# Kernel tuning notes

Hardware: AMD Instinct MI355X
Metric: run time of the kernel (lower is better)

## Reference

```python
import jax, jax.numpy as jnp
import numpy as np

# Detect() defaults from the source
NUM_CLASSES = 2
TOP_K = 750          # max detections returned per class
NMS_TOP_K = 5000     # candidates considered by NMS
NMS_THRESH = 0.3
CONF_THRESH = 0.05
VAR0, VAR1 = 0.1, 0.2  # prior box variances


def decode(loc, priors):
    # loc, priors: [P,4]; priors in (cx,cy,w,h); returns corner boxes [P,4]
    xy = priors[:, :2] + loc[:, :2] * VAR0 * priors[:, 2:]
    wh = priors[:, 2:] * jnp.exp(loc[:, 2:] * VAR1)
    x1y1 = xy - wh * 0.5
    x2y2 = x1y1 + wh
    return jnp.concatenate([x1y1, x2y2], axis=1)


def nms_single(boxes, scores):
    # boxes [P,4], scores [P] -> kept rows [TOP_K,5] = (score, x1,y1,x2,y2)
    s = jnp.where(scores > CONF_THRESH, scores, -1.0)
    top_s, top_i = jax.lax.top_k(s, NMS_TOP_K)   # restrict to best nms_top_k candidates
    cb = boxes[top_i]                             # [K,4] candidate boxes
    area = (cb[:, 2] - cb[:, 0]) * (cb[:, 3] - cb[:, 1])
    ar = jnp.arange(NMS_TOP_K)

    def step(s_cur, _):
        i = jnp.argmax(s_cur)                     # highest-scoring unsuppressed box
        sc = s_cur[i]
        ok = sc > 0.0                             # any valid candidate left?
        b = cb[i]
        xx1 = jnp.maximum(cb[:, 0], b[0])
        yy1 = jnp.maximum(cb[:, 1], b[1])
        xx2 = jnp.minimum(cb[:, 2], b[2])
        yy2 = jnp.minimum(cb[:, 3], b[3])
        inter = jnp.clip(xx2 - xx1, 0.0) * jnp.clip(yy2 - yy1, 0.0)
        union = area - inter + area[i]
        iou = inter / union
        supp = (iou > NMS_THRESH) | (ar == i)     # suppress overlapping + self
        s_next = jnp.where(ok & supp, -1.0, s_cur)
        row = jnp.where(ok, jnp.concatenate([sc[None], b]), jnp.zeros(5, boxes.dtype))
        return s_next, row

    _, rows = jax.lax.scan(step, top_s, None, length=TOP_K)
    return rows  # [TOP_K, 5]


def setup_inputs() -> dict:
    key = jax.random.key(0)
    k1, k2, k3 = jax.random.split(key, 3)
    B, P = 8, 136500
    loc_data = jax.random.normal(k1, (B, P, 4), jnp.float32)
    conf_data = jax.random.normal(k2, (B, P, 2), jnp.float32)
    u = jax.random.uniform(k3, (P, 4), jnp.float32)
    # priors: cx,cy in (0,1); w,h small positive (normalized coords)
    prior_data = jnp.concatenate([u[:, :2], u[:, 2:] * 0.1 + 0.01], axis=1)
    return {"loc_data": loc_data, "conf_data": conf_data, "prior_data": prior_data}


def reference(loc_data, conf_data, prior_data):
    B = loc_data.shape[0]
    conf = jax.nn.softmax(conf_data, axis=-1)                    # [B,P,2]
    boxes = jax.vmap(lambda l: decode(l, prior_data))(loc_data)  # [B,P,4]
    rows = jax.vmap(nms_single)(boxes, conf[:, :, 1])            # [B,TOP_K,5]
    out = jnp.zeros((B, NUM_CLASSES, TOP_K, 5), loc_data.dtype)  # class 0 = background, all zeros
    out = out.at[:, 1].set(rows)
    return out
```

## Files before the change

### kernel.cpp

```cpp
#include <hip/hip_runtime.h>
#include <stdint.h>

#pragma clang fp contract(off)

#define NPRI   136500
#define BATCH  8
#define NMS_K  5000
#define NKPAD  5120
#define TOPK   750
#define SORT_N 8192
#define HBINS  1024
#define HOFF   0x3D40
#define MROW   80
#define CNTSTRIDE 32
#define CUT    32

typedef unsigned long long u64;

__device__ __forceinline__ u64 shfl64(u64 v, int src) {
    int lo = __shfl((int)(unsigned)(v & 0xffffffffull), src);
    int hi = __shfl((int)(unsigned)(v >> 32), src);
    return ((u64)(unsigned)hi << 32) | (u64)(unsigned)lo;
}
__device__ __forceinline__ u64 shfl64_xor(u64 v, int m) {
    int lo = __shfl_xor((int)(unsigned)(v & 0xffffffffull), m);
    int hi = __shfl_xor((int)(unsigned)(v >> 32), m);
    return ((u64)(unsigned)hi << 32) | (u64)(unsigned)lo;
}

__device__ __forceinline__ bool iou_sup(float4 c4, float aj,
                                        float4 rbx, float ra) {
    float xx1 = fmaxf(c4.x, rbx.x);
    float yy1 = fmaxf(c4.y, rbx.y);
    float xx2 = fminf(c4.z, rbx.z);
    float yy2 = fminf(c4.w, rbx.w);
    float iw = fmaxf(xx2 - xx1, 0.0f);
    float ih = fmaxf(yy2 - yy1, 0.0f);
    float inter = iw * ih;
    float uni = (aj - inter) + ra;
    float u = fmaf(-0.3f, uni, inter);
    float d = fmaf(-1.4901161193847656e-8f, uni, u);
    return d > 0.0f;
}
__device__ __forceinline__ u64 iou_word(float4 c4, float aj,
                                        float4 rbx, float ra) {
    return __ballot(iou_sup(c4, aj, rbx, ra));
}

__device__ __forceinline__ u64 diag_mask(u64 word, int sh) {
    if (sh >= 0)
        word &= (sh >= 63) ? 0ull : (~0ull << (sh + 1));
    return word;
}

__device__ u64 row_word_slow(const float4* __restrict__ cbp,
                             const float* __restrict__ cap,
                             float4 rbx, float ra, int W) {
    int jbase = W << 6;
    u64 word = 0ull;
    for (int jj = 0; jj < 64; ++jj) {
        int jc = min(jbase + jj, NMS_K - 1);
        if (iou_sup(cbp[jc], cap[jc], rbx, ra)) word |= (1ull << jj);
    }
    return word;
}

__global__ __launch_bounds__(256) void score_hist_kernel(
        const float* __restrict__ conf, unsigned int* __restrict__ hist,
        float* __restrict__ sraw) {
    int b = blockIdx.y;
    __shared__ unsigned int h[HBINS];
    for (int i = threadIdx.x; i < HBINS; i += 256) h[i] = 0;
    __syncthreads();
    for (int p = blockIdx.x * 256 + threadIdx.x; p < NPRI; p += 64 * 256) {
        float2 c = ((const float2*)conf)[(size_t)b * NPRI + p];
        float m  = fmaxf(c.x, c.y);
        float e0 = expf(c.x - m), e1 = expf(c.y - m);
        float s  = e1 / (e0 + e1);
        sraw[(size_t)b * NPRI + p] = s;
        if (s > 0.05f) {
            int bin = (int)(__float_as_uint(s) >> 16) - HOFF;
            bin = min(max(bin, 0), HBINS - 1);
            atomicAdd(&h[bin], 1u);
        }
    }
    __syncthreads();
    for (int i = threadIdx.x; i < HBINS; i += 256) {
        unsigned int v = h[i];
        if (v) atomicAdd(&hist[b * HBINS + i], v);
    }
}

__global__ __launch_bounds__(256) void compact_kernel(
        const float* __restrict__ sraw, const unsigned int* __restrict__ hist,
        u64* __restrict__ keys, unsigned int* __restrict__ cnt) {
    int b = blockIdx.y;
    int tid = threadIdx.x;
    int lane = tid & 63;
    __shared__ u64 buf[2304];
    __shared__ unsigned int hsum[256];
    __shared__ int best_sh;
    __shared__ unsigned int nloc;
    __shared__ unsigned int base_sh;
    const unsigned int* hb = hist + b * HBINS;
    int t4 = tid * 4;
    unsigned int h0 = hb[t4], h1 = hb[t4 + 1], h2 = hb[t4 + 2], h3 = hb[t4 + 3];
    hsum[tid] = h0 + h1 + h2 + h3;
    if (tid == 0) { best_sh = 0; nloc = 0; }
    __syncthreads();
    for (int o = 1; o < 256; o <<= 1) {
        unsigned int add = (tid + o < 256) ? hsum[tid + o] : 0u;
        __syncthreads();
        hsum[tid] += add;
        __syncthreads();
    }
    unsigned int nxt = (tid + 1 < 256) ? hsum[tid + 1] : 0u;
    unsigned int s3 = h3 + nxt;
    unsigned int s2 = h2 + s3;
    unsigned int s1 = h1 + s2;
    unsigned int s0 = h0 + s1;
    int cand = -1;
    if (s3 >= (unsigned)NMS_K) cand = t4 + 3;
    else if (s2 >= (unsigned)NMS_K) cand = t4 + 2;
    else if (s1 >= (unsigned)NMS_K) cand = t4 + 1;
    else if (s0 >= (unsigned)NMS_K) cand = t4;
    if (cand > 0) atomicMax(&best_sh, cand);
    __syncthreads();
    int tb = best_sh;
    for (int p = blockIdx.x * 256 + tid; p < NPRI; p += 64 * 256) {
        float s = sraw[(size_t)b * NPRI + p];
        bool pass = false;
        unsigned int bits = 0;
        if (s > 0.05f) {
            bits = __float_as_uint(s);
            int bin = (int)(bits >> 16) - HOFF;
            bin = min(max(bin, 0), HBINS - 1);
            pass = (bin >= tb);
        }
        u64 bal = __ballot(pass);
        int rank = (int)__popcll(bal & ((1ull << lane) - 1ull));
        unsigned int wbase = 0;
        if (lane == 0 && bal)
            wbase = atomicAdd(&nloc, (unsigned)__popcll(bal));
        wbase = (unsigned)__shfl((int)wbase, 0);
        if (pass)
            buf[wbase + rank] = ((u64)bits << 32) | (u64)(~(unsigned int)p);
    }
    __syncthreads();
    unsigned int tot = nloc;
    if (tid == 0)
        base_sh = tot ? atomicAdd(&cnt[b * CNTSTRIDE], tot) : 0u;
    __syncthreads();
    unsigned int base = base_sh;
    for (unsigned int i = tid; i < tot; i += 256) {
        unsigned int pos = base + i;
        if (pos < SORT_N)
            keys[(size_t)b * SORT_N + pos] = buf[i];
    }
}

__global__ __launch_bounds__(512) void sort2k_kernel(
        const u64* __restrict__ keys, u64* __restrict__ keys2,
        const unsigned int* __restrict__ cnt) {
    int b = blockIdx.y, c = blockIdx.x;
    int tid = threadIdx.x;
    int n = min((int)cnt[b * CNTSTRIDE], SORT_N);
    int base = c * 2048;
    if (base >= n) {
        for (int i = tid; i < 2048; i += 512)
            keys2[(size_t)b * SORT_N + base + i] = 0ull;
        return;
    }
    __shared__ u64 k[2048];
    for (int i = tid; i < 2048; i += 512)
        k[i] = (base + i < n) ? keys[(size_t)b * SORT_N + base + i] : 0ull;
    __syncthreads();
    for (int kk = 2; kk <= 2048; kk <<= 1) {
        bool top = (kk == 2048);
        for (int j = kk >> 1; j > 0; j >>= 1) {
            for (int i = tid; i < 2048; i += 512) {
                int ixj = i ^ j;
                if (ixj > i) {
                    u64 a = k[i], v = k[ixj];
                    bool desc = top || ((i & kk) == 0);
                    if (desc ? (a < v) : (a > v)) { k[i] = v; k[ixj] = a; }
                }
            }
            __syncthreads();
        }
    }
    for (int i = tid; i < 2048; i += 512)
        keys2[(size_t)b * SORT_N + base + i] = k[i];
}

__global__ __launch_bounds__(256) void merge1_kernel(
        const u64* __restrict__ keys2, u64* __restrict__ keys) {
    int b = blockIdx.y;
    int o = blockIdx.x * 256 + threadIdx.x;
    int pair = o >> 12;
    int oo = o & 4095;
    const u64* A  = keys2 + (size_t)b * SORT_N + pair * 4096;
    const u64* Bp = A + 2048;
    int lo = max(0, oo - 2048), hi = min(oo, 2048);
    while (lo < hi) {
        int mid = (lo + hi + 1) >> 1;
        bool ok = (oo - mid >= 2048) || (A[mid - 1] >= Bp[oo - mid]);
        if (ok) lo = mid; else hi = mid - 1;
    }
    int i = lo, j = oo - lo;
    u64 v;
    if (j >= 2048) v = A[i];
    else if (i >= 2048) v = Bp[j];
    else v = (A[i] >= Bp[j]) ? A[i] : Bp[j];
    keys[(size_t)b * SORT_N + pair * 4096 + oo] = v;
}

__global__ __launch_bounds__(256) void merge2_decode_kernel(
        const u64* __restrict__ keys,
        const float* __restrict__ loc, const float* __restrict__ priors,
        float* __restrict__ cscore, float* __restrict__ cbox,
        float* __restrict__ carea) {
    int b = blockIdx.y;
    int o = blockIdx.x * 256 + threadIdx.x;
    const u64* A  = keys + (size_t)b * SORT_N;
    const u64* Bp = A + 4096;
    int lo = max(0, o - 4096), hi = min(o, 4096);
    while (lo < hi) {
        int mid = (lo + hi + 1) >> 1;
        bool ok = (o - mid >= 4096) || (A[mid - 1] >= Bp[o - mid]);
        if (ok) lo = mid; else hi = mid - 1;
    }
    int i = lo, j = o - lo;
    u64 key;
    if (j >= 4096) key = A[i];
    else if (i >= 4096) key = Bp[j];
    else key = (A[i] >= Bp[j]) ? A[i] : Bp[j];
    if (o >= NMS_K) return;
    float sc; int idx;
    if (key != 0ull) {
        sc  = __uint_as_float((unsigned int)(key >> 32));
        idx = (int)(~(unsigned int)key);
    } else { sc = -1.0f; idx = 0; }
    cscore[b * NMS_K + o] = sc;
    float x1 = 0.f, y1 = 0.f, x2 = 0.f, y2 = 0.f, ar = 0.f;
    if (key != 0ull) {
        const float* l  = loc + ((size_t)b * NPRI + idx) * 4;
        const float* pr = priors + (size_t)idx * 4;
        float lx = l[0], ly = l[1], lw = l[2], lh = l[3];
        float pcx = pr[0], pcy = pr[1], pw = pr[2], ph = pr[3];
        float cx = pcx + (lx * 0.1f) * pw;
        float cy = pcy + (ly * 0.1f) * ph;
        float wd = pw * expf(lw * 0.2f);
        float ht = ph * expf(lh * 0.2f);
        x1 = cx - wd * 0.5f;  y1 = cy - ht * 0.5f;
        x2 = x1 + wd;         y2 = y1 + ht;
        ar = (x2 - x1) * (y2 - y1);
    }
    float* cb = cbox + ((size_t)b * NMS_K + o) * 4;
    cb[0] = x1; cb[1] = y1; cb[2] = x2; cb[3] = y2;
    carea[b * NMS_K + o] = ar;
}

__global__ __launch_bounds__(256, 4) void maskbuild_kernel(
        const float* __restrict__ cbox, const float* __restrict__ carea,
        u64* __restrict__ M) {
    int b   = blockIdx.y;
    int bid = blockIdx.x;
    int wgq, rb;
    if (bid >= 380) { wgq = 19; rb = bid - 380; }
    else {
        int w = (int)((sqrtf((float)(4 * bid + 5)) - 1.0f) * 0.5f);
        while (w * (w + 1) > bid) w--;
        while ((w + 1) * (w + 2) <= bid) w++;
        wgq = w; rb = bid - w * (w + 1);
    }
    int tid  = threadIdx.x;
    int lane = tid & 63;
    int wv   = __builtin_amdgcn_readfirstlane(tid >> 6);
    int w0   = wgq * 4;
    int rowbase = rb * 128;

    __shared__ float4 rbox[128];
    __shared__ float  rarea[128];
    if (tid < 128) {
        int i  = rowbase + tid;
        int ic = min(i, NMS_K - 1);
        rbox[tid]  = ((const float4*)cbox)[(size_t)b * NMS_K + ic];
        rarea[tid] = carea[(size_t)b * NMS_K + ic];
    }
    const float4* __restrict__ cbp = (const float4*)cbox + (size_t)b * NMS_K;
    const float*  __restrict__ cap = carea + (size_t)b * NMS_K;
    int j0 = w0 * 64 + lane;
    float4 c4_0 = cbp[min(j0,       NMS_K - 1)];
    float4 c4_1 = cbp[min(j0 +  64, NMS_K - 1)];
    float4 c4_2 = cbp[min(j0 + 128, NMS_K - 1)];
    float4 c4_3 = cbp[min(j0 + 192, NMS_K - 1)];
    float aj0 = cap[min(j0,       NMS_K - 1)];
    float aj1 = cap[min(j0 +  64, NMS_K - 1)];
    float aj2 = cap[min(j0 + 128, NMS_K - 1)];
    float aj3 = cap[min(j0 + 192, NMS_K - 1)];
    __syncthreads();

    int lr0 = 32 * wv;
    int rglob0 = rowbase + lr0;
    if (rglob0 >= NMS_K) return;

    u64* __restrict__ Mb = M + (size_t)b * NKPAD * MROW;

    if (rglob0 + 31 < w0 * 64) {
#pragma unroll 2
        for (int q = 0; q < 32; q += 2) {
            int lr = lr0 + q;
            float4 rb0 = rbox[lr], rb1 = rbox[lr + 1];
            float  ra0 = rarea[lr], ra1 = rarea[lr + 1];
            u64 A0 = iou_word(c4_0, aj0, rb0, ra0);
            u64 B0 = iou_word(c4_0, aj0, rb1, ra1);
            u64 A1 = iou_word(c4_1, aj1, rb0, ra0);
            u64 B1 = iou_word(c4_1, aj1, rb1, ra1);
            u64 A2 = iou_word(c4_2, aj2, rb0, ra0);
            u64 B2 = iou_word(c4_2, aj2, rb1, ra1);
            u64 A3 = iou_word(c4_3, aj3, rb0, ra0);
            u64 B3 = iou_word(c4_3, aj3, rb1, ra1);
            int row0 = rglob0 + q;
            if (lane == 0) {
                u64* d0 = Mb + (size_t)row0 * MROW + w0;
                ((ulonglong2*)d0)[0] = make_ulonglong2(A0, A1);
                ((ulonglong2*)d0)[1] = make_ulonglong2(A2, A3);
                u64* d1 = d0 + MROW;
                ((ulonglong2*)d1)[0] = make_ulonglong2(B0, B1);
                ((ulonglong2*)d1)[1] = make_ulonglong2(B2, B3);
            }
        }
    } else {
        int nrows = min(32, NMS_K - rglob0);
        int sh_base = rglob0 - w0 * 64;
#pragma unroll 2
        for (int q = 0; q < nrows; q += 2) {
            int lr = lr0 + q;
            float4 rb0 = rbox[lr], rb1 = rbox[lr + 1];
            float  ra0 = rarea[lr], ra1 = rarea[lr + 1];
            u64 A0 = iou_word(c4_0, aj0, rb0, ra0);
            u64 B0 = iou_word(c4_0, aj0, rb1, ra1);
            u64 A1 = iou_word(c4_1, aj1, rb0, ra0);
            u64 B1 = iou_word(c4_1, aj1, rb1, ra1);
            u64 A2 = iou_word(c4_2, aj2, rb0, ra0);
            u64 B2 = iou_word(c4_2, aj2, rb1, ra1);
            u64 A3 = iou_word(c4_3, aj3, rb0, ra0);
            u64 B3 = iou_word(c4_3, aj3, rb1, ra1);
            int sh = sh_base + q;
            A0 = diag_mask(A0, sh);       B0 = diag_mask(B0, sh + 1);
            A1 = diag_mask(A1, sh - 64);  B1 = diag_mask(B1, sh - 63);
            A2 = diag_mask(A2, sh - 128); B2 = diag_mask(B2, sh - 127);
            A3 = diag_mask(A3, sh - 192); B3 = diag_mask(B3, sh - 191);
            int row0 = rglob0 + q;
            if (lane == 0) {
                u64* d0 = Mb + (size_t)row0 * MROW + w0;
                ((ulonglong2*)d0)[0] = make_ulonglong2(A0, A1);
                ((ulonglong2*)d0)[1] = make_ulonglong2(A2, A3);
                u64* d1 = d0 + MROW;
                ((ulonglong2*)d1)[0] = make_ulonglong2(B0, B1);
                ((ulonglong2*)d1)[1] = make_ulonglong2(B2, B3);
            }
        }
    }
}

__global__ __launch_bounds__(1024) void maskscan_kernel(
        const float* __restrict__ cscore, const float* __restrict__ cbox,
        const float* __restrict__ carea,
        const unsigned int* __restrict__ cnt, const u64* __restrict__ M,
        float* __restrict__ out) {
    int b = blockIdx.x;
    int tid = threadIdx.x, lane = tid & 63, wv = tid >> 6;
    int nv = min((int)cnt[b * CNTSTRIDE], NMS_K);
    const u64* MB = M + (size_t)b * NKPAD * MROW;
    const float4* __restrict__ cbp = (const float4*)cbox + (size_t)b * NMS_K;
    const float*  __restrict__ cap = carea + (size_t)b * NMS_K;
    float* outb = out + (size_t)b * 2 * TOPK * 5;
    __shared__ unsigned int supp4[4];
    __shared__ u64 dbuf[2][64];
    __shared__ short allp[TOPK];
    __shared__ int emitted_sh;
    for (int i = tid; i < 2 * TOPK * 5; i += 1024) outb[i] = 0.f;
    if (tid < 4) supp4[tid] = 0u;
    if (tid == 0) emitted_sh = 0;
    if (wv == 1) dbuf[0][lane] = MB[(size_t)lane * MROW];
    __syncthreads();
    int emitted = 0;
    int nwords = (nv + 63) >> 6;
    u64 colw_prev = 0ull;
    u64 pickprev  = 0ull;
    for (int w = 0; w < nwords; w++) {
        int par = w & 1;
        if (wv == 0) {
            u64 colw;
            if (w + 1 < CUT) {
                colw = MB[(size_t)(w * 64 + lane) * MROW + (w + 1)];
            } else {
                int rc = min(w * 64 + lane, NMS_K - 1);
                colw = row_word_slow(cbp, cap, cbp[rc], cap[rc], w + 1);
            }
            u64 D = dbuf[par][lane];
            u64 sup = ((u64)supp4[2 * par + 1] << 32) | (u64)supp4[2 * par];
            if (lane == 0) {
                supp4[2 * par] = 0u;
                supp4[2 * par + 1] = 0u;
            }
            u64 x = ((pickprev >> lane) & 1ull) ? colw_prev : 0ull;
#pragma unroll
            for (int m = 1; m < 64; m <<= 1) x |= shfl64_xor(x, m);
            sup |= x;
            int base = w * 64, rem = nv - base;
            u64 valid = (rem >= 64) ? ~0ull : ((1ull << rem) - 1ull);
            u64 alive = valid & ~sup;
            u64 nz = __ballot(D != 0ull);
            u64 pickmask = 0ull;
            while (alive) {
                u64 blockers = alive & nz;
                if (!blockers) { pickmask |= alive; break; }
                int nb = __builtin_ctzll(blockers);
                u64 mle = (nb >= 63) ? ~0ull : ((1ull << (nb + 1)) - 1ull);
                pickmask |= alive & mle;
                u64 rw = shfl64(D, nb);
                alive &= ~mle;
                alive &= ~rw;
            }
            int room = TOPK - emitted;
            int pc = __popcll(pickmask);
            while (pc > room) {
                pickmask &= ~(1ull << (63 - __builtin_clzll(pickmask)));
                pc--;
            }
            if (lane == 0) emitted_sh = emitted + pc;
            if ((pickmask >> lane) & 1ull) {
                int rank = (int)__popcll(pickmask & ((1ull << lane) - 1ull));
                allp[emitted + rank] = (short)(base + lane);
            }
            pickprev = pickmask;
            colw_prev = colw;
        } else if (wv == 1) {
            if (w + 1 < nwords) {
                int W = w + 1;
                u64 dpre;
                if (W < CUT) {
                    dpre = MB[(size_t)(W * 64 + lane) * MROW + W];
                } else {
                    int rc = min(W * 64 + lane, NMS_K - 1);
                    dpre = diag_mask(
                        row_word_slow(cbp, cap, cbp[rc], cap[rc], W), lane);
                }
                dbuf[W & 1][lane] = dpre;
            }
        } else {
            int i = (wv - 2) * 64 + lane;
            u64 v = 0ull;
            if (i < emitted) {
                int pr = allp[i];
                if (w + 1 < CUT)
                    v = MB[(size_t)pr * MROW + (w + 1)];
                else
                    v = row_word_slow(cbp, cap, cbp[pr], cap[pr], w + 1);
            }
#pragma unroll
            for (int m = 1; m < 64; m <<= 1) v |= shfl64_xor(v, m);
            if (lane == 0 && v) {
                atomicOr(&supp4[2 * (par ^ 1)],     (unsigned int)v);
                atomicOr(&supp4[2 * (par ^ 1) + 1], (unsigned int)(v >> 32));
            }
        }
        __syncthreads();
        emitted = emitted_sh;
        if (emitted >= TOPK) break;
    }
    for (int t = tid; t < emitted; t += 1024) {
        int p = allp[t];
        float sc  = cscore[b * NMS_K + p];
        float4 bx = ((const float4*)cbox)[(size_t)b * NMS_K + p];
        float* o = outb + (size_t)(TOPK + t) * 5;
        o[0] = sc; o[1] = bx.x; o[2] = bx.y; o[3] = bx.z; o[4] = bx.w;
    }
}

extern "C" void kernel_launch(void* const* d_in, const int* in_sizes, int n_in,
                              void* d_out, int out_size, void* d_ws, size_t ws_size,
                              hipStream_t stream) {
    const float* loc    = (const float*)d_in[0];
    const float* conf   = (const float*)d_in[1];
    const float* priors = (const float*)d_in[2];
    float* out = (float*)d_out;

    char* ws = (char*)d_ws;
    size_t off = 0;
    unsigned int* hist = (unsigned int*)(ws + off);   off += (size_t)BATCH * HBINS * 4;
    unsigned int* cnt  = (unsigned int*)(ws + off);   off += (size_t)BATCH * CNTSTRIDE * 4;
    size_t zero_bytes = off;
    u64* keys  = (u64*)(ws + off);                    off += (size_t)BATCH * SORT_N * 8;
    u64* keys2 = (u64*)(ws + off);                    off += (size_t)BATCH * SORT_N * 8;
    float* cscore = (float*)(ws + off);               off += (size_t)BATCH * NMS_K * 4;
    float* cbox   = (float*)(ws + off);               off += (size_t)BATCH * NMS_K * 16;
    float* carea  = (float*)(ws + off);               off += (size_t)BATCH * NMS_K * 4;
    u64* M = (u64*)(ws + off);                        off += (size_t)BATCH * NKPAD * MROW * 8;
    float* sraw = (float*)M;

    hipMemsetAsync(d_ws, 0, zero_bytes, stream);

    score_hist_kernel<<<dim3(64, BATCH), 256, 0, stream>>>(conf, hist, sraw);
    compact_kernel<<<dim3(64, BATCH), 256, 0, stream>>>(sraw, hist, keys, cnt);
    sort2k_kernel<<<dim3(4, BATCH), 512, 0, stream>>>(keys, keys2, cnt);
    merge1_kernel<<<dim3(32, BATCH), 256, 0, stream>>>(keys2, keys);
    merge2_decode_kernel<<<dim3(20, BATCH), 256, 0, stream>>>(keys, loc, priors, cscore, cbox, carea);
    maskbuild_kernel<<<dim3(72, BATCH), 256, 0, stream>>>(cbox, carea, M);
    maskscan_kernel<<<BATCH, 1024, 0, stream>>>(cscore, cbox, carea, cnt, M, out);
}
```

Before: 185.0 us.

## Replace shared-memory bitonic sort with wave-shuffle sort plus merge-path passes

The 2048-element per-block bitonic sort, which needed a block barrier at every one of its many stages, is replaced. Each wave now sorts 64-element chunks in registers with xor shuffles, and five merge-path passes ping-pong between two shared buffers to combine them, with one barrier per pass. This cuts the number of block-wide synchronisations and shared-memory round trips. In exchange it adds binary-search work per output element and doubles the shared memory used per block.

```diff
diff --git a/kernel.cpp b/kernel.cpp
--- a/kernel.cpp
+++ b/kernel.cpp
@@ -159,11 +159,13 @@
     }
 }
 
-__global__ __launch_bounds__(512) void sort2k_kernel(
+__global__ __launch_bounds__(512) void sortmerge2k_kernel(
         const u64* __restrict__ keys, u64* __restrict__ keys2,
         const unsigned int* __restrict__ cnt) {
     int b = blockIdx.y, c = blockIdx.x;
     int tid = threadIdx.x;
+    int lane = tid & 63;
+    int wv = tid >> 6;
     int n = min((int)cnt[b * CNTSTRIDE], SORT_N);
     int base = c * 2048;
     if (base >= n) {
@@ -172,25 +174,51 @@
         return;
     }
     __shared__ u64 k[2048];
+    __shared__ u64 k2[2048];
+    for (int ch = wv; ch < 32; ch += 8) {
+        int idx = base + ch * 64 + lane;
+        u64 v = (idx < n) ? keys[(size_t)b * SORT_N + idx] : 0ull;
+#pragma unroll
+        for (int kk = 2; kk <= 64; kk <<= 1) {
+#pragma unroll
+            for (int j = kk >> 1; j > 0; j >>= 1) {
+                u64 o = shfl64_xor(v, j);
+                bool low  = (lane & j) == 0;
+                bool desc = (lane & kk) == 0;
+                u64 mx = (v >= o) ? v : o;
+                u64 mn = (v >= o) ? o : v;
+                v = desc ? (low ? mx : mn) : (low ? mn : mx);
+            }
+        }
+        k[ch * 64 + lane] = v;
+    }
+    __syncthreads();
+    u64* src = k;
+    u64* dst = k2;
+    for (int L = 64; L < 2048; L <<= 1) {
+        for (int o = tid; o < 2048; o += 512) {
+            int pair = o / (2 * L);
+            int oo = o - pair * 2 * L;
+            const u64* A  = src + pair * 2 * L;
+            const u64* Bp = A + L;
+            int lo = max(0, oo - L), hi = min(oo, L);
+            while (lo < hi) {
+                int mid = (lo + hi + 1) >> 1;
+                bool ok = (oo - mid >= L) || (A[mid - 1] >= Bp[oo - mid]);
+                if (ok) lo = mid; else hi = mid - 1;
+            }
+            int i = lo, j = oo - lo;
+            u64 v;
+            if (j >= L) v = A[i];
+            else if (i >= L) v = Bp[j];
+            else v = (A[i] >= Bp[j]) ? A[i] : Bp[j];
+            dst[o] = v;
+        }
+        __syncthreads();
+        u64* t = src; src = dst; dst = t;
+    }
     for (int i = tid; i < 2048; i += 512)
-        k[i] = (base + i < n) ? keys[(size_t)b * SORT_N + base + i] : 0ull;
-    __syncthreads();
-    for (int kk = 2; kk <= 2048; kk <<= 1) {
-        bool top = (kk == 2048);
-        for (int j = kk >> 1; j > 0; j >>= 1) {
-            for (int i = tid; i < 2048; i += 512) {
-                int ixj = i ^ j;
-                if (ixj > i) {
-                    u64 a = k[i], v = k[ixj];
-                    bool desc = top || ((i & kk) == 0);
-                    if (desc ? (a < v) : (a > v)) { k[i] = v; k[ixj] = a; }
-                }
-            }
-            __syncthreads();
-        }
-    }
-    for (int i = tid; i < 2048; i += 512)
-        keys2[(size_t)b * SORT_N + base + i] = k[i];
+        keys2[(size_t)b * SORT_N + base + i] = src[i];
 }
 
 __global__ __launch_bounds__(256) void merge1_kernel(
@@ -506,7 +534,7 @@
 
     score_hist_kernel<<<dim3(64, BATCH), 256, 0, stream>>>(conf, hist, sraw);
     compact_kernel<<<dim3(64, BATCH), 256, 0, stream>>>(sraw, hist, keys, cnt);
-    sort2k_kernel<<<dim3(4, BATCH), 512, 0, stream>>>(keys, keys2, cnt);
+    sortmerge2k_kernel<<<dim3(4, BATCH), 512, 0, stream>>>(keys, keys2, cnt);
     merge1_kernel<<<dim3(32, BATCH), 256, 0, stream>>>(keys2, keys);
     merge2_decode_kernel<<<dim3(20, BATCH), 256, 0, stream>>>(keys, loc, priors, cscore, cbox, carea);
     maskbuild_kernel<<<dim3(72, BATCH), 256, 0, stream>>>(cbox, carea, M);
```

New measurement: 165.9 us. -10.4%, faster.
